# Optimization experiments

Measured on AMD Instinct MI355X. Metric: run time of the kernel, lower is better.

Reference implementation:

```python
import jax, jax.numpy as jnp
import numpy as np

B, T, I, H, A = 128, 1024, 128, 256, 40


def setup_inputs() -> dict:
    key = jax.random.key(0)
    ks = jax.random.split(key, 10)
    s_ih = 1.0 / np.sqrt(H)
    return {
        "x": jax.random.normal(ks[0], (B, T, I), dtype=jnp.float32),
        "W_ih": jax.random.uniform(ks[1], (3 * H, I), minval=-s_ih, maxval=s_ih, dtype=jnp.float32),
        "W_hh": jax.random.uniform(ks[2], (3 * H, H), minval=-s_ih, maxval=s_ih, dtype=jnp.float32),
        "b_ih": jax.random.uniform(ks[3], (3 * H,), minval=-s_ih, maxval=s_ih, dtype=jnp.float32),
        "b_hh": jax.random.uniform(ks[4], (3 * H,), minval=-s_ih, maxval=s_ih, dtype=jnp.float32),
        "wv_W": jax.random.normal(ks[5], (A, H), dtype=jnp.float32) * 0.05,
        "wv_b": jnp.zeros((A,), dtype=jnp.float32),
        "wu": jax.random.uniform(ks[6], (A,), dtype=jnp.float32),
        "h2o_W": jax.random.normal(ks[7], (1, H), dtype=jnp.float32) * 0.05,
        "h2o_b": jnp.zeros((1,), dtype=jnp.float32),
    }


def _gru_outputs(x, W_ih, W_hh, b_ih, b_hh):
    # Precompute input-side gate projections for all timesteps: [B,T,3H]
    gx = jnp.einsum("bti,gi->btg", x, W_ih) + b_ih
    h0 = jnp.zeros((x.shape[0], H), dtype=x.dtype)

    def step(h, gx_t):
        gh = h @ W_hh.T + b_hh                      # [B,3H]
        xr, xz, xn = jnp.split(gx_t, 3, axis=-1)    # torch gate order r,z,n
        hr, hz, hn = jnp.split(gh, 3, axis=-1)
        r = jax.nn.sigmoid(xr + hr)
        z = jax.nn.sigmoid(xz + hz)
        n = jnp.tanh(xn + r * hn)
        h_new = (1.0 - z) * n + z * h
        return h_new, h_new

    _, hs = jax.lax.scan(step, h0, jnp.swapaxes(gx, 0, 1))  # hs: [T,B,H]
    return jnp.swapaxes(hs, 0, 1)  # [B,T,H]


def reference(x, W_ih, W_hh, b_ih, b_hh, wv_W, wv_b, wu, h2o_W, h2o_b):
    outputs = _gru_outputs(x, W_ih, W_hh, b_ih, b_hh)          # [B,T,H]
    um = jnp.tanh(jnp.einsum("bth,ah->bta", outputs, wv_W) + wv_b)  # [B,T,A]
    alpha = jax.nn.softmax(um @ wu, axis=1)                    # [B,T]
    context = jnp.einsum("bt,bth->bh", alpha, outputs)         # [B,H]
    # dropout_layer is identity in eval mode
    out = context @ h2o_W.T + h2o_b                            # [B,1]
    return out
```

## Files before the change

### kernel.cpp

```cpp
#include <hip/hip_runtime.h>


#define B_ 128
#define T_ 1024
#define I_ 128
#define H_ 256
#define G_ 768
#define A_ 40

typedef _Float16 f16;
typedef _Float16 f16x2 __attribute__((ext_vector_type(2)));

__device__ __forceinline__ float fdot2(unsigned a, unsigned b, float c){
#if __has_builtin(__builtin_amdgcn_fdot2)
  return __builtin_amdgcn_fdot2(__builtin_bit_cast(f16x2, a),
                                __builtin_bit_cast(f16x2, b), c, false);
#else
  f16x2 av = __builtin_bit_cast(f16x2, a), bv = __builtin_bit_cast(f16x2, b);
  return c + (float)av.x * (float)bv.x + (float)av.y * (float)bv.y;
#endif
}

__device__ __forceinline__ float2 h2f(unsigned u){
  f16x2 h = __builtin_bit_cast(f16x2, u);
  return make_float2((float)h.x, (float)h.y);
}
__device__ __forceinline__ unsigned f2h2(float a, float b){
  f16x2 h; h.x = (f16)a; h.y = (f16)b;
  return __builtin_bit_cast(unsigned, h);
}
__device__ __forceinline__ float sigm_(float x){ return 1.f / (1.f + __expf(-x)); }
__device__ __forceinline__ float tanh_(float x){ return 1.f - 2.f / (__expf(2.f * x) + 1.f); }

__global__ __launch_bounds__(256) void k_prep_w(const float* __restrict__ W,
                                                unsigned* __restrict__ Wp){
  int idx = blockIdx.x * 256 + threadIdx.x;
  int d   = idx >> 9;
  int col = idx & 511;
  int g = col >> 1, sub = col & 1;
  int c = d >> 6, p = d & 63;
  int r = g + 256 * c;
  int k = sub * 128 + 2 * p;
  Wp[(size_t)d * 512 + col] = f2h2(W[r * 256 + k], W[r * 256 + k + 1]);
}

__global__ __launch_bounds__(256) void k_gx(const float* __restrict__ x,
                                            const float* __restrict__ wih,
                                            const float* __restrict__ bih,
                                            unsigned* __restrict__ gx){
  __shared__ float Al[64 * 68];
  __shared__ float Bl[64 * 68];
  const int tid = threadIdx.x;
  const int m0 = blockIdx.x * 64, n0 = blockIdx.y * 64;
  const int ar = tid >> 4, bc = tid & 15;
  float acc[4][4] = {{0.f}};

  for (int kh = 0; kh < 2; ++kh){
    __syncthreads();
    #pragma unroll
    for (int u = 0; u < 4; ++u){
      int idx = tid + 256 * u;
      int row = idx >> 4;
      int kq  = idx & 15;
      float4 va = *(const float4*)(x   + (size_t)(m0 + row) * I_ + kh * 64 + kq * 4);
      float4 vb = *(const float4*)(wih + (size_t)(n0 + row) * I_ + kh * 64 + kq * 4);
      Al[(kq*4+0)*68 + row] = va.x; Al[(kq*4+1)*68 + row] = va.y;
      Al[(kq*4+2)*68 + row] = va.z; Al[(kq*4+3)*68 + row] = va.w;
      Bl[(kq*4+0)*68 + row] = vb.x; Bl[(kq*4+1)*68 + row] = vb.y;
      Bl[(kq*4+2)*68 + row] = vb.z; Bl[(kq*4+3)*68 + row] = vb.w;
    }
    __syncthreads();
    for (int k = 0; k < 64; ++k){
      float4 a4 = *(const float4*)(Al + k * 68 + ar * 4);
      float4 b4 = *(const float4*)(Bl + k * 68 + bc * 4);
      acc[0][0] += a4.x*b4.x; acc[0][1] += a4.x*b4.y; acc[0][2] += a4.x*b4.z; acc[0][3] += a4.x*b4.w;
      acc[1][0] += a4.y*b4.x; acc[1][1] += a4.y*b4.y; acc[1][2] += a4.y*b4.z; acc[1][3] += a4.y*b4.w;
      acc[2][0] += a4.z*b4.x; acc[2][1] += a4.z*b4.y; acc[2][2] += a4.z*b4.z; acc[2][3] += a4.z*b4.w;
      acc[3][0] += a4.w*b4.x; acc[3][1] += a4.w*b4.y; acc[3][2] += a4.w*b4.z; acc[3][3] += a4.w*b4.w;
    }
  }

  float bn[4];
  #pragma unroll
  for (int j = 0; j < 4; ++j) bn[j] = bih[n0 + bc * 4 + j];
  #pragma unroll
  for (int i = 0; i < 4; ++i){
    int m = m0 + ar * 4 + i;
    uint2 st;
    st.x = f2h2(acc[i][0] + bn[0], acc[i][1] + bn[1]);
    st.y = f2h2(acc[i][2] + bn[2], acc[i][3] + bn[3]);
    *(uint2*)(gx + (size_t)m * (G_ / 2) + n0 / 2 + bc * 2) = st;
  }
}

__global__ __launch_bounds__(512, 2) void k_gru(const unsigned* __restrict__ Wp,
                                                unsigned* __restrict__ gx,
                                                const float* __restrict__ bhh,
                                                int unused){
  __shared__ uint4 HB4[2][32];
  const int tid = threadIdx.x;
  const int b = blockIdx.x;
  const int g = tid >> 1, sub = tid & 1;

  unsigned w[192];
  #pragma unroll
  for (int d = 0; d < 192; ++d) w[d] = Wp[d * 512 + tid];

  float br = 0.f, bz = 0.f, bn_ = 0.f, hprev = 0.f;
  if (sub == 0){ br = bhh[g]; bz = bhh[H_ + g]; bn_ = bhh[2 * H_ + g]; }
  if (tid < 32) HB4[0][tid] = make_uint4(0, 0, 0, 0);
  __syncthreads();

  f16* gxp = (f16*)gx + (size_t)b * T_ * G_;

  float xr = 0.f, xz = 0.f, xn = 0.f;
  if (sub == 0){ xr = (float)gxp[g]; xz = (float)gxp[H_ + g]; xn = (float)gxp[2 * H_ + g]; }

  int buf = 0;
  for (int t = 0; t < T_; ++t){
    float nr = 0.f, nz = 0.f, nn = 0.f;
    if (sub == 0 && t < T_ - 1){
      const f16* nx = gxp + (size_t)(t + 1) * G_;
      nr = (float)nx[g]; nz = (float)nx[H_ + g]; nn = (float)nx[2 * H_ + g];
    }

    float a0 = 0.f, a1 = 0.f, a2 = 0.f;
    #pragma unroll
    for (int i = 0; i < 16; ++i){
      uint4 hc = HB4[buf][sub * 16 + i];
      a0 = fdot2(w[      i*4+0], hc.x, a0); a0 = fdot2(w[      i*4+1], hc.y, a0);
      a0 = fdot2(w[      i*4+2], hc.z, a0); a0 = fdot2(w[      i*4+3], hc.w, a0);
      a1 = fdot2(w[ 64 + i*4+0], hc.x, a1); a1 = fdot2(w[ 64 + i*4+1], hc.y, a1);
      a1 = fdot2(w[ 64 + i*4+2], hc.z, a1); a1 = fdot2(w[ 64 + i*4+3], hc.w, a1);
      a2 = fdot2(w[128 + i*4+0], hc.x, a2); a2 = fdot2(w[128 + i*4+1], hc.y, a2);
      a2 = fdot2(w[128 + i*4+2], hc.z, a2); a2 = fdot2(w[128 + i*4+3], hc.w, a2);
    }
    a0 += __shfl_xor(a0, 1);
    a1 += __shfl_xor(a1, 1);
    a2 += __shfl_xor(a2, 1);

    if (sub == 0){
      float rg = sigm_(xr + a0 + br);
      float zg = sigm_(xz + a1 + bz);
      float ng = tanh_(xn + rg * (a2 + bn_));
      float hn = (1.f - zg) * ng + zg * hprev;
      hprev = hn;
      f16 hh = (f16)hn;
      ((f16*)HB4[buf ^ 1])[g] = hh;
      gxp[(size_t)t * G_ + g] = hh;
      xr = nr; xz = nz; xn = nn;
    }
    __syncthreads();
    buf ^= 1;
  }
}

__global__ __launch_bounds__(256) void k_score(const f16* __restrict__ outs,
                                               const float* __restrict__ wvW,
                                               const float* __restrict__ wvb,
                                               const float* __restrict__ wu,
                                               float* __restrict__ s){
  __shared__ uint4 OT[32 * 33];
  __shared__ float WV[A_ * 260];
  const int tid = threadIdx.x;
  const int m0 = blockIdx.x * 32;

  #pragma unroll
  for (int u = 0; u < 4; ++u){
    int idx = tid + 256 * u;
    int row = idx >> 5, col = idx & 31;
    OT[row * 33 + col] = *(const uint4*)(outs + (size_t)(m0 + row) * G_ + col * 8);
  }
  #pragma unroll
  for (int u = 0; u < 10; ++u){
    int f = tid + 256 * u;
    int a = f >> 6, k4 = f & 63;
    float4 v = *(const float4*)(wvW + a * 256 + k4 * 4);
    *(float4*)(WV + a * 260 + k4 * 4) = v;
  }
  __syncthreads();

  const int m = tid >> 3, aq = tid & 7;
  float acc[5] = {0.f, 0.f, 0.f, 0.f, 0.f};
  for (int i = 0; i < 32; ++i){
    uint4 oc = OT[m * 33 + i];
    float2 o01 = h2f(oc.x), o23 = h2f(oc.y), o45 = h2f(oc.z), o67 = h2f(oc.w);
    #pragma unroll
    for (int sa = 0; sa < 5; ++sa){
      int a = aq + sa * 8;
      const float* wr = &WV[a * 260 + i * 8];
      float4 w0 = *(const float4*)wr;
      float4 w1 = *(const float4*)(wr + 4);
      acc[sa] += o01.x*w0.x + o01.y*w0.y + o23.x*w0.z + o23.y*w0.w
               + o45.x*w1.x + o45.y*w1.y + o67.x*w1.z + o67.y*w1.w;
    }
  }
  float sp = 0.f;
  #pragma unroll
  for (int sa = 0; sa < 5; ++sa){
    int a = aq + sa * 8;
    sp += wu[a] * tanh_(acc[sa] + wvb[a]);
  }
  sp += __shfl_xor(sp, 1);
  sp += __shfl_xor(sp, 2);
  sp += __shfl_xor(sp, 4);
  if (aq == 0) s[m0 + m] = sp;
}

__global__ __launch_bounds__(256) void k_ctx(const f16* __restrict__ outs,
                                             const float* __restrict__ s,
                                             const float* __restrict__ h2oW,
                                             const float* __restrict__ h2ob,
                                             float* __restrict__ out){
  __shared__ float AL[T_];
  __shared__ float red[8];
  const int tid = threadIdx.x;
  const int b = blockIdx.x;
  const float* sb = s + (size_t)b * T_;

  float v0 = sb[tid], v1 = sb[tid + 256], v2 = sb[tid + 512], v3 = sb[tid + 768];
  float mx = fmaxf(fmaxf(v0, v1), fmaxf(v2, v3));
  #pragma unroll
  for (int msk = 1; msk < 64; msk <<= 1) mx = fmaxf(mx, __shfl_xor(mx, msk));
  if ((tid & 63) == 0) red[tid >> 6] = mx;
  __syncthreads();
  mx = fmaxf(fmaxf(red[0], red[1]), fmaxf(red[2], red[3]));

  float e0 = __expf(v0 - mx), e1 = __expf(v1 - mx), e2 = __expf(v2 - mx), e3 = __expf(v3 - mx);
  float zs = e0 + e1 + e2 + e3;
  #pragma unroll
  for (int msk = 1; msk < 64; msk <<= 1) zs += __shfl_xor(zs, msk);
  if ((tid & 63) == 0) red[4 + (tid >> 6)] = zs;
  __syncthreads();
  float invZ = 1.f / (red[4] + red[5] + red[6] + red[7]);
  AL[tid] = e0 * invZ; AL[tid + 256] = e1 * invZ;
  AL[tid + 512] = e2 * invZ; AL[tid + 768] = e3 * invZ;
  __syncthreads();

  const f16* ob = outs + (size_t)b * T_ * G_;
  float acc = 0.f;
  for (int t = 0; t < T_; t += 4){
    acc += AL[t + 0] * (float)ob[(size_t)(t + 0) * G_ + tid];
    acc += AL[t + 1] * (float)ob[(size_t)(t + 1) * G_ + tid];
    acc += AL[t + 2] * (float)ob[(size_t)(t + 2) * G_ + tid];
    acc += AL[t + 3] * (float)ob[(size_t)(t + 3) * G_ + tid];
  }
  __syncthreads();
  float val = acc * h2oW[tid];
  #pragma unroll
  for (int msk = 1; msk < 64; msk <<= 1) val += __shfl_xor(val, msk);
  if ((tid & 63) == 0) red[tid >> 6] = val;
  __syncthreads();
  if (tid == 0) out[b] = red[0] + red[1] + red[2] + red[3] + h2ob[0];
}

extern "C" void kernel_launch(void* const* d_in, const int* in_sizes, int n_in,
                              void* d_out, int out_size, void* d_ws, size_t ws_size,
                              hipStream_t stream){
  const float* x    = (const float*)d_in[0];
  const float* wih  = (const float*)d_in[1];
  const float* whh  = (const float*)d_in[2];
  const float* bih  = (const float*)d_in[3];
  const float* bhh  = (const float*)d_in[4];
  const float* wvW  = (const float*)d_in[5];
  const float* wvb  = (const float*)d_in[6];
  const float* wu   = (const float*)d_in[7];
  const float* h2oW = (const float*)d_in[8];
  const float* h2ob = (const float*)d_in[9];
  float* out = (float*)d_out;

  char* ws = (char*)d_ws;
  float*    s  = (float*)ws;
  unsigned* Wp = (unsigned*)(ws + 524288);
  unsigned* gx = (unsigned*)(ws + 917504);

  k_prep_w<<<384, 256, 0, stream>>>(whh, Wp);
  k_gx<<<dim3((B_ * T_) / 64, G_ / 64), 256, 0, stream>>>(x, wih, bih, gx);
  k_gru<<<B_, 512, 0, stream>>>(Wp, gx, bhh, 0);
  k_score<<<(B_ * T_) / 32, 256, 0, stream>>>((const f16*)gx, wvW, wvb, wu, s);
  k_ctx<<<B_, 256, 0, stream>>>((const f16*)gx, s, h2oW, h2ob, out);
}
```

Before: 1.999 ms.

## Assign one GRU gate row per thread and use fp16 dot2 in input projection

The recurrent kernel now runs 768 threads per batch row, one per gate row, each holding its full 256-wide weight row in registers (128 packed halves). This replaces the earlier layout of 512 threads with split-K plus a shuffle. The z and n gate pre-activations are passed through shared memory, which adds a second barrier per timestep but removes the shuffles and lets all threads share the dot-product work. The weight prep kernel is changed to match the new layout. Separately, the input-projection GEMM now packs x and W_ih to fp16 pairs in shared memory and uses fdot2, which halves shared traffic and FMA count at some loss of precision.

```diff
diff --git a/kernel.cpp b/kernel.cpp
--- a/kernel.cpp
+++ b/kernel.cpp
@@ -35,21 +35,17 @@
 __global__ __launch_bounds__(256) void k_prep_w(const float* __restrict__ W,
                                                 unsigned* __restrict__ Wp){
   int idx = blockIdx.x * 256 + threadIdx.x;
-  int d   = idx >> 9;
-  int col = idx & 511;
-  int g = col >> 1, sub = col & 1;
-  int c = d >> 6, p = d & 63;
-  int r = g + 256 * c;
-  int k = sub * 128 + 2 * p;
-  Wp[(size_t)d * 512 + col] = f2h2(W[r * 256 + k], W[r * 256 + k + 1]);
+  int r = idx >> 7;
+  int d = idx & 127;
+  Wp[(size_t)d * G_ + r] = f2h2(W[r * 256 + 2 * d], W[r * 256 + 2 * d + 1]);
 }
 
 __global__ __launch_bounds__(256) void k_gx(const float* __restrict__ x,
                                             const float* __restrict__ wih,
                                             const float* __restrict__ bih,
                                             unsigned* __restrict__ gx){
-  __shared__ float Al[64 * 68];
-  __shared__ float Bl[64 * 68];
+  __shared__ __align__(16) unsigned Au[32 * 68];
+  __shared__ __align__(16) unsigned Bu[32 * 68];
   const int tid = threadIdx.x;
   const int m0 = blockIdx.x * 64, n0 = blockIdx.y * 64;
   const int ar = tid >> 4, bc = tid & 15;
@@ -64,19 +60,24 @@
       int kq  = idx & 15;
       float4 va = *(const float4*)(x   + (size_t)(m0 + row) * I_ + kh * 64 + kq * 4);
       float4 vb = *(const float4*)(wih + (size_t)(n0 + row) * I_ + kh * 64 + kq * 4);
-      Al[(kq*4+0)*68 + row] = va.x; Al[(kq*4+1)*68 + row] = va.y;
-      Al[(kq*4+2)*68 + row] = va.z; Al[(kq*4+3)*68 + row] = va.w;
-      Bl[(kq*4+0)*68 + row] = vb.x; Bl[(kq*4+1)*68 + row] = vb.y;
-      Bl[(kq*4+2)*68 + row] = vb.z; Bl[(kq*4+3)*68 + row] = vb.w;
-    }
-    __syncthreads();
-    for (int k = 0; k < 64; ++k){
-      float4 a4 = *(const float4*)(Al + k * 68 + ar * 4);
-      float4 b4 = *(const float4*)(Bl + k * 68 + bc * 4);
-      acc[0][0] += a4.x*b4.x; acc[0][1] += a4.x*b4.y; acc[0][2] += a4.x*b4.z; acc[0][3] += a4.x*b4.w;
-      acc[1][0] += a4.y*b4.x; acc[1][1] += a4.y*b4.y; acc[1][2] += a4.y*b4.z; acc[1][3] += a4.y*b4.w;
-      acc[2][0] += a4.z*b4.x; acc[2][1] += a4.z*b4.y; acc[2][2] += a4.z*b4.z; acc[2][3] += a4.z*b4.w;
-      acc[3][0] += a4.w*b4.x; acc[3][1] += a4.w*b4.y; acc[3][2] += a4.w*b4.z; acc[3][3] += a4.w*b4.w;
+      Au[(2*kq  ) * 68 + row] = f2h2(va.x, va.y);
+      Au[(2*kq+1) * 68 + row] = f2h2(va.z, va.w);
+      Bu[(2*kq  ) * 68 + row] = f2h2(vb.x, vb.y);
+      Bu[(2*kq+1) * 68 + row] = f2h2(vb.z, vb.w);
+    }
+    __syncthreads();
+    #pragma unroll 8
+    for (int kp = 0; kp < 32; ++kp){
+      uint4 a4 = *(const uint4*)(Au + kp * 68 + ar * 4);
+      uint4 b4 = *(const uint4*)(Bu + kp * 68 + bc * 4);
+      acc[0][0]=fdot2(a4.x,b4.x,acc[0][0]); acc[0][1]=fdot2(a4.x,b4.y,acc[0][1]);
+      acc[0][2]=fdot2(a4.x,b4.z,acc[0][2]); acc[0][3]=fdot2(a4.x,b4.w,acc[0][3]);
+      acc[1][0]=fdot2(a4.y,b4.x,acc[1][0]); acc[1][1]=fdot2(a4.y,b4.y,acc[1][1]);
+      acc[1][2]=fdot2(a4.y,b4.z,acc[1][2]); acc[1][3]=fdot2(a4.y,b4.w,acc[1][3]);
+      acc[2][0]=fdot2(a4.z,b4.x,acc[2][0]); acc[2][1]=fdot2(a4.z,b4.y,acc[2][1]);
+      acc[2][2]=fdot2(a4.z,b4.z,acc[2][2]); acc[2][3]=fdot2(a4.z,b4.w,acc[2][3]);
+      acc[3][0]=fdot2(a4.w,b4.x,acc[3][0]); acc[3][1]=fdot2(a4.w,b4.y,acc[3][1]);
+      acc[3][2]=fdot2(a4.w,b4.z,acc[3][2]); acc[3][3]=fdot2(a4.w,b4.w,acc[3][3]);
     }
   }
 
@@ -93,65 +94,61 @@
   }
 }
 
-__global__ __launch_bounds__(512, 2) void k_gru(const unsigned* __restrict__ Wp,
+__global__ __launch_bounds__(768, 3) void k_gru(const unsigned* __restrict__ Wp,
                                                 unsigned* __restrict__ gx,
-                                                const float* __restrict__ bhh,
-                                                int unused){
-  __shared__ uint4 HB4[2][32];
+                                                const float* __restrict__ bhh){
+  __shared__ uint4 Hc4[32];
+  __shared__ float GH[512];
   const int tid = threadIdx.x;
   const int b = blockIdx.x;
-  const int g = tid >> 1, sub = tid & 1;
-
-  unsigned w[192];
-  #pragma unroll
-  for (int d = 0; d < 192; ++d) w[d] = Wp[d * 512 + tid];
-
-  float br = 0.f, bz = 0.f, bn_ = 0.f, hprev = 0.f;
-  if (sub == 0){ br = bhh[g]; bz = bhh[H_ + g]; bn_ = bhh[2 * H_ + g]; }
-  if (tid < 32) HB4[0][tid] = make_uint4(0, 0, 0, 0);
-  __syncthreads();
+
+  unsigned w[128];
+  #pragma unroll
+  for (int d = 0; d < 128; ++d) w[d] = Wp[(size_t)d * G_ + tid];
+
+  const float bias = bhh[tid];
+  float hprev = 0.f;
+  if (tid < 32) Hc4[tid] = make_uint4(0, 0, 0, 0);
 
   f16* gxp = (f16*)gx + (size_t)b * T_ * G_;
 
-  float xr = 0.f, xz = 0.f, xn = 0.f;
-  if (sub == 0){ xr = (float)gxp[g]; xz = (float)gxp[H_ + g]; xn = (float)gxp[2 * H_ + g]; }
-
-  int buf = 0;
+  float xcur  = (float)gxp[tid];
+  float xncur = (tid < 256) ? (float)gxp[512 + tid] : 0.f;
+  __syncthreads();
+
   for (int t = 0; t < T_; ++t){
-    float nr = 0.f, nz = 0.f, nn = 0.f;
-    if (sub == 0 && t < T_ - 1){
-      const f16* nx = gxp + (size_t)(t + 1) * G_;
-      nr = (float)nx[g]; nz = (float)nx[H_ + g]; nn = (float)nx[2 * H_ + g];
-    }
-
-    float a0 = 0.f, a1 = 0.f, a2 = 0.f;
+    float xnext = 0.f, xnnext = 0.f;
+    if (t + 1 < T_){
+      xnext = (float)gxp[(size_t)(t + 1) * G_ + tid];
+      if (tid < 256) xnnext = (float)gxp[(size_t)(t + 1) * G_ + 512 + tid];
+    }
+
+    float a0 = 0.f, a1 = 0.f;
     #pragma unroll
-    for (int i = 0; i < 16; ++i){
-      uint4 hc = HB4[buf][sub * 16 + i];
-      a0 = fdot2(w[      i*4+0], hc.x, a0); a0 = fdot2(w[      i*4+1], hc.y, a0);
-      a0 = fdot2(w[      i*4+2], hc.z, a0); a0 = fdot2(w[      i*4+3], hc.w, a0);
-      a1 = fdot2(w[ 64 + i*4+0], hc.x, a1); a1 = fdot2(w[ 64 + i*4+1], hc.y, a1);
-      a1 = fdot2(w[ 64 + i*4+2], hc.z, a1); a1 = fdot2(w[ 64 + i*4+3], hc.w, a1);
-      a2 = fdot2(w[128 + i*4+0], hc.x, a2); a2 = fdot2(w[128 + i*4+1], hc.y, a2);
-      a2 = fdot2(w[128 + i*4+2], hc.z, a2); a2 = fdot2(w[128 + i*4+3], hc.w, a2);
-    }
-    a0 += __shfl_xor(a0, 1);
-    a1 += __shfl_xor(a1, 1);
-    a2 += __shfl_xor(a2, 1);
-
-    if (sub == 0){
-      float rg = sigm_(xr + a0 + br);
-      float zg = sigm_(xz + a1 + bz);
-      float ng = tanh_(xn + rg * (a2 + bn_));
-      float hn = (1.f - zg) * ng + zg * hprev;
-      hprev = hn;
-      f16 hh = (f16)hn;
-      ((f16*)HB4[buf ^ 1])[g] = hh;
-      gxp[(size_t)t * G_ + g] = hh;
-      xr = nr; xz = nz; xn = nn;
-    }
-    __syncthreads();
-    buf ^= 1;
+    for (int j = 0; j < 32; ++j){
+      uint4 hv = Hc4[j];
+      a0 = fdot2(w[4*j+0], hv.x, a0); a1 = fdot2(w[4*j+1], hv.y, a1);
+      a0 = fdot2(w[4*j+2], hv.z, a0); a1 = fdot2(w[4*j+3], hv.w, a1);
+    }
+    float a = a0 + a1;
+
+    if (tid >= 512)      GH[tid - 256] = a + bias;
+    else if (tid >= 256) GH[tid - 256] = sigm_(a + bias + xcur);
+    __syncthreads();
+
+    if (tid < 256){
+      float rg = sigm_(xcur + a + bias);
+      float zg = GH[tid];
+      float ng = tanh_(xncur + rg * GH[256 + tid]);
+      float h  = (1.f - zg) * ng + zg * hprev;
+      hprev = h;
+      f16 hh = (f16)h;
+      ((f16*)Hc4)[tid] = hh;
+      gxp[(size_t)t * G_ + tid] = hh;
+      xncur = xnnext;
+    }
+    xcur = xnext;
+    __syncthreads();
   }
 }
 
@@ -276,7 +273,7 @@
 
   k_prep_w<<<384, 256, 0, stream>>>(whh, Wp);
   k_gx<<<dim3((B_ * T_) / 64, G_ / 64), 256, 0, stream>>>(x, wih, bih, gx);
-  k_gru<<<B_, 512, 0, stream>>>(Wp, gx, bhh, 0);
+  k_gru<<<B_, 768, 0, stream>>>(Wp, gx, bhh);
   k_score<<<(B_ * T_) / 32, 256, 0, stream>>>((const f16*)gx, wvW, wvb, wu, s);
   k_ctx<<<B_, 256, 0, stream>>>((const f16*)gx, s, h2oW, h2ob, out);
 }
```

New measurement: 1.636 ms. 1.22x faster.
